# Kernel tuning notes

Measured on AMD Instinct MI355X. Metric: run time of the kernel, lower is better.

The kernel has to match this reference:

```python
import jax, jax.numpy as jnp
import numpy as np

B, T, D, FC, H = 256, 256, 512, 512, 512
EPS = 1e-5

def setup_inputs() -> dict:
    key = jax.random.key(0)
    ks = jax.random.split(key, 13)
    s = lambda k, shape, fan: jax.random.normal(k, shape, jnp.float32) * (1.0 / np.sqrt(fan))
    return {
        "inputs": jax.random.normal(ks[0], (B, T, D), jnp.float32),
        "hidden_state": jax.random.normal(ks[1], (B, H), jnp.float32),
        "episode_starts": jax.random.randint(ks[2], (B, T), 0, 2, jnp.int32),
        "ln_gamma": jnp.ones((D,), jnp.float32),
        "ln_beta": jnp.zeros((D,), jnp.float32),
        "w_in": s(ks[3], (FC, D), D),
        "b_in": jnp.zeros((FC,), jnp.float32),
        "w_ih": s(ks[4], (3 * H, FC), FC),
        "b_ih": jnp.zeros((3 * H,), jnp.float32),
        "w_hh": s(ks[5], (3 * H, H), H),
        "b_hh": jnp.zeros((3 * H,), jnp.float32),
        "w_out": s(ks[6], (H, H), H),
        "b_out": jnp.zeros((H,), jnp.float32),
    }

def reference(inputs, hidden_state, episode_starts, ln_gamma, ln_beta,
              w_in, b_in, w_ih, b_ih, w_hh, b_hh, w_out, b_out):
    # LayerNorm + fc_in + input-side GRU gates have no recurrence -> batch over time.
    mu = jnp.mean(inputs, axis=-1, keepdims=True)
    var = jnp.mean(jnp.square(inputs - mu), axis=-1, keepdims=True)
    xn = (inputs - mu) * jax.lax.rsqrt(var + EPS) * ln_gamma + ln_beta
    x = jax.nn.relu(jnp.einsum('btd,fd->btf', xn, w_in) + b_in)        # [B,T,FC]
    gi = jnp.einsum('btf,gf->btg', x, w_ih) + b_ih                      # [B,T,3H]
    mask = 1.0 - episode_starts.astype(jnp.float32)                     # [B,T]

    def step(h, inp):
        gi_t, m_t = inp                    # gi_t: [B,3H], m_t: [B]
        h = h * m_t[:, None]               # masked reset
        gh = h @ w_hh.T + b_hh             # [B,3H]
        ir, iz, inn = jnp.split(gi_t, 3, axis=-1)
        hr, hz, hn = jnp.split(gh, 3, axis=-1)
        r = jax.nn.sigmoid(ir + hr)
        z = jax.nn.sigmoid(iz + hz)
        n = jnp.tanh(inn + r * hn)
        h_new = (1.0 - z) * n + z * h
        return h_new, h_new

    h_last, hs = jax.lax.scan(step, hidden_state,
                              (gi.transpose(1, 0, 2), mask.T))          # hs: [T,B,H]
    outputs = jax.nn.relu(jnp.einsum('tbh,oh->tbo', hs, w_out) + b_out)
    return outputs.transpose(1, 0, 2), h_last
```

## Files before the change

### kernel.cpp

```cpp
#include <hip/hip_runtime.h>
#include <hip/hip_bf16.h>

#define B_  256
#define T_  256
#define D_  512
#define H_  512
#define G3_ 1536

typedef __attribute__((ext_vector_type(8))) short bf16x8;
typedef __attribute__((ext_vector_type(4))) float f32x4;
typedef __attribute__((ext_vector_type(8))) unsigned short u16x8;
typedef __attribute__((ext_vector_type(4))) unsigned short u16x4;

__device__ inline void gload_lds16(const void* g, void* l) {
  __builtin_amdgcn_global_load_lds((const __attribute__((address_space(1))) void*)g,
                                   (__attribute__((address_space(3))) void*)l,
                                   16, 0, 0);
}

__device__ inline unsigned short f2bu(float f) {
  __hip_bfloat16 h = __float2bfloat16(f);
  return *reinterpret_cast<unsigned short*>(&h);
}
__device__ inline float bu2f(unsigned short u) {
  return __uint_as_float((unsigned)u << 16);
}

__device__ inline bf16x8 ld16_sys(const void* p) {
  bf16x8 r;
  asm volatile("global_load_dwordx4 %0, %1, off sc0 sc1" : "=v"(r) : "v"(p) : "memory");
  return r;
}
__device__ inline void st8_sys(void* p, u16x4 v) {
  asm volatile("global_store_dwordx2 %0, %1, off sc0 sc1" :: "v"(p), "v"(v) : "memory");
}
__device__ inline void st4_sys(void* p, unsigned v) {
  asm volatile("global_store_dword %0, %1, off sc0 sc1" :: "v"(p), "v"(v) : "memory");
}
__device__ inline unsigned ld4_sys_wait(const void* p) {
  unsigned r;
  asm volatile("global_load_dword %0, %1, off sc0 sc1\n\ts_waitcnt vmcnt(0)"
               : "=v"(r) : "v"(p) : "memory");
  return r;
}
__device__ inline void waitvm0() { asm volatile("s_waitcnt vmcnt(0)" ::: "memory"); }

__global__ void prep_kernel(const float* __restrict__ w_in, const float* __restrict__ w_ih,
                            const float* __restrict__ w_out,
                            __hip_bfloat16* __restrict__ wib, __hip_bfloat16* __restrict__ whb,
                            __hip_bfloat16* __restrict__ wob, unsigned int* __restrict__ ctrs) {
  int i = blockIdx.x * 256 + threadIdx.x;
  if (i < D_ * D_)  wib[i] = __float2bfloat16(w_in[i]);
  if (i < G3_ * D_) whb[i] = __float2bfloat16(w_ih[i]);
  if (i < H_ * H_)  wob[i] = __float2bfloat16(w_out[i]);
  if (i < 1024) ctrs[i] = 0u;
}

__global__ __launch_bounds__(512) void ln_kernel(const float* __restrict__ x,
                                                 const float* __restrict__ gamma,
                                                 const float* __restrict__ beta,
                                                 __hip_bfloat16* __restrict__ xn) {
  long row = (long)blockIdx.x * 8 + (threadIdx.x >> 6);
  int lane = threadIdx.x & 63;
  const float4* rp = (const float4*)(x + row * D_ + lane * 8);
  float4 v0 = rp[0], v1 = rp[1];
  float s  = v0.x + v0.y + v0.z + v0.w + v1.x + v1.y + v1.z + v1.w;
  float sq = v0.x*v0.x + v0.y*v0.y + v0.z*v0.z + v0.w*v0.w
           + v1.x*v1.x + v1.y*v1.y + v1.z*v1.z + v1.w*v1.w;
  #pragma unroll
  for (int off = 1; off < 64; off <<= 1) { s += __shfl_xor(s, off); sq += __shfl_xor(sq, off); }
  float mean = s * (1.0f / D_);
  float var  = sq * (1.0f / D_) - mean * mean;
  float rstd = rsqrtf(var + 1e-5f);
  const float4* gp = (const float4*)(gamma + lane * 8);
  const float4* bp = (const float4*)(beta + lane * 8);
  float4 g0 = gp[0], g1 = gp[1], bb0 = bp[0], bb1 = bp[1];
  float vv[8] = {v0.x, v0.y, v0.z, v0.w, v1.x, v1.y, v1.z, v1.w};
  float gg[8] = {g0.x, g0.y, g0.z, g0.w, g1.x, g1.y, g1.z, g1.w};
  float bt[8] = {bb0.x, bb0.y, bb0.z, bb0.w, bb1.x, bb1.y, bb1.z, bb1.w};
  u16x8 ov;
  #pragma unroll
  for (int i = 0; i < 8; ++i) ov[i] = f2bu((vv[i] - mean) * rstd * gg[i] + bt[i]);
  *(u16x8*)(xn + row * D_ + lane * 8) = ov;
}

template<int ACT, int OUTBF>
__global__ __launch_bounds__(256) void gemm_bt(const __hip_bfloat16* __restrict__ A,
                                               const __hip_bfloat16* __restrict__ W,
                                               const float* __restrict__ bias,
                                               void* __restrict__ Cout,
                                               int M, int N, int K) {
  __shared__ __hip_bfloat16 As[128 * 64];
  __shared__ __hip_bfloat16 Ws[128 * 64];
  int tid  = threadIdx.x;
  int lane = tid & 63;
  int wave = tid >> 6;
  long row0 = (long)blockIdx.y * 128;
  long col0 = (long)blockIdx.x * 128;
  int qm = (wave >> 1) * 64, qn = (wave & 1) * 64;
  int lr = lane & 15, lk = (lane >> 4) * 8;
  f32x4 acc[4][4];
  #pragma unroll
  for (int mt = 0; mt < 4; ++mt)
    #pragma unroll
    for (int nt = 0; nt < 4; ++nt) acc[mt][nt] = {0.f, 0.f, 0.f, 0.f};

  for (int k0 = 0; k0 < K; k0 += 64) {
    #pragma unroll
    for (int i = 0; i < 4; ++i) {
      int e = i * 2048 + tid * 8;
      int r = e >> 6, c = e & 63;
      gload_lds16(A + (row0 + r) * K + k0 + c, (char*)As + 2 * e);
      gload_lds16(W + (col0 + r) * K + k0 + c, (char*)Ws + 2 * e);
    }
    __syncthreads();
    #pragma unroll
    for (int kc = 0; kc < 2; ++kc) {
      int kb = kc * 32 + lk;
      bf16x8 af[4], wf[4];
      #pragma unroll
      for (int mt = 0; mt < 4; ++mt) af[mt] = *(const bf16x8*)&As[(qm + mt * 16 + lr) * 64 + kb];
      #pragma unroll
      for (int nt = 0; nt < 4; ++nt) wf[nt] = *(const bf16x8*)&Ws[(qn + nt * 16 + lr) * 64 + kb];
      #pragma unroll
      for (int mt = 0; mt < 4; ++mt)
        #pragma unroll
        for (int nt = 0; nt < 4; ++nt)
          acc[mt][nt] = __builtin_amdgcn_mfma_f32_16x16x32_bf16(af[mt], wf[nt], acc[mt][nt], 0, 0, 0);
    }
    __syncthreads();
  }
  int r0 = (lane >> 4) * 4;
  #pragma unroll
  for (int nt = 0; nt < 4; ++nt) {
    long col = col0 + qn + nt * 16 + lr;
    float bv = bias[col];
    #pragma unroll
    for (int mt = 0; mt < 4; ++mt) {
      #pragma unroll
      for (int q = 0; q < 4; ++q) {
        long row = row0 + qm + mt * 16 + r0 + q;
        float v = acc[mt][nt][q] + bv;
        if (ACT) v = fmaxf(v, 0.0f);
        if (OUTBF) ((__hip_bfloat16*)Cout)[row * N + col] = __float2bfloat16(v);
        else       ((float*)Cout)[row * N + col] = v;
      }
    }
  }
}

__global__ __launch_bounds__(256) void scan_kernel(const __hip_bfloat16* __restrict__ gi,
                                                   const float* __restrict__ hidden,
                                                   const int* __restrict__ ep,
                                                   const float* __restrict__ w_hh,
                                                   const float* __restrict__ b_hh,
                                                   __hip_bfloat16* __restrict__ hs,
                                                   __hip_bfloat16* __restrict__ hbuf,
                                                   float* __restrict__ h_last,
                                                   unsigned int* __restrict__ flags) {
  __shared__ __hip_bfloat16 Wl[96][520];
  __shared__ float ghs[32][100];
  __shared__ f32x4 hown4[256];
  __shared__ unsigned epm[256];
  __shared__ float bhh[96];

  const int tid = threadIdx.x;
  const int bg = blockIdx.x & 7;
  const int nb = blockIdx.x >> 3;
  const int rb0 = bg * 32;
  const int j0 = nb * 32;
  unsigned* gflags = flags + bg * 16;

  for (int idx = tid; idx < 96 * 512; idx += 256) {
    int row = idx >> 9, c = idx & 511;
    int g = row >> 5, jj = row & 31;
    Wl[row][c] = __float2bfloat16(w_hh[(size_t)(g * 512 + j0 + jj) * 512 + c]);
  }
  if (tid < 96) bhh[tid] = b_hh[(tid >> 5) * 512 + j0 + (tid & 31)];
  {
    unsigned m = 0;
    for (int b = 0; b < 32; ++b)
      m |= (ep[(rb0 + b) * T_ + tid] != 0) ? (1u << b) : 0u;
    epm[tid] = m;
  }

  {
    int b = tid >> 3, jb = (tid & 7) * 4;
    const float4 hv = *(const float4*)(hidden + (size_t)(rb0 + b) * 512 + j0 + jb);
    f32x4 h4 = {hv.x, hv.y, hv.z, hv.w};
    hown4[tid] = h4;
    u16x4 hb;
    #pragma unroll
    for (int k = 0; k < 4; ++k) hb[k] = f2bu(h4[k]);
    st8_sys(hbuf + (size_t)(bg * 2) * 32 * 512 + b * 512 + j0 + jb, hb);
  }
  waitvm0();
  __syncthreads();
  if (tid == 0) st4_sys(gflags + nb, 1u);

  const int lane = tid & 63;
  const int wave = tid >> 6;
  const int mt = wave >> 1;
  const int npair = wave & 1;
  const int lr = lane & 15;
  const int asub = lane >> 4;
  const int arow = mt * 16 + lr;
  const int gb = tid >> 3, gjb = (tid & 7) * 4;

  for (int t = 0; t < T_; ++t) {
    const u16x4* gp = (const u16x4*)(gi + ((size_t)(rb0 + gb) * T_ + t) * G3_ + j0 + gjb);
    u16x4 gr4 = gp[0], gz4 = gp[128], gn4 = gp[256];

    if (wave == 0) {
      unsigned want = (unsigned)(t + 1);
      for (;;) {
        unsigned f = ld4_sys_wait(gflags + (lane & 15));
        if (__all((int)(f >= want))) break;
        __builtin_amdgcn_s_sleep(1);
      }
    }
    __syncthreads();

    const __hip_bfloat16* hsrc = hbuf + (size_t)(bg * 2 + (t & 1)) * 32 * 512;
    const char* abase = (const char*)(hsrc + (size_t)arow * 512 + asub * 8);
    bf16x8 af[16];
    #pragma unroll
    for (int kc = 0; kc < 16; ++kc) af[kc] = ld16_sys(abase + kc * 64);
    bool masked = ((epm[t] >> arow) & 1u) != 0u;
    waitvm0();
    __builtin_amdgcn_sched_barrier(0);
    if (masked) {
      #pragma unroll
      for (int kc = 0; kc < 16; ++kc) af[kc] = (bf16x8){0, 0, 0, 0, 0, 0, 0, 0};
    }

    f32x4 acc[3];
    #pragma unroll
    for (int i = 0; i < 3; ++i) acc[i] = (f32x4){0.f, 0.f, 0.f, 0.f};
    #pragma unroll
    for (int kc = 0; kc < 16; ++kc) {
      #pragma unroll
      for (int i = 0; i < 3; ++i) {
        bf16x8 bf = *(const bf16x8*)&Wl[npair * 48 + i * 16 + lr][kc * 32 + asub * 8];
        acc[i] = __builtin_amdgcn_mfma_f32_16x16x32_bf16(af[kc], bf, acc[i], 0, 0, 0);
      }
    }
    #pragma unroll
    for (int i = 0; i < 3; ++i)
      #pragma unroll
      for (int q = 0; q < 4; ++q)
        ghs[mt * 16 + asub * 4 + q][npair * 48 + i * 16 + lr] = acc[i][q];
    __syncthreads();

    __hip_bfloat16* hdst = hbuf + (size_t)(bg * 2 + ((t + 1) & 1)) * 32 * 512;
    unsigned em = epm[t];
    float live = ((em >> gb) & 1u) ? 0.0f : 1.0f;
    f32x4 ghr = *(const f32x4*)&ghs[gb][gjb];
    f32x4 ghz = *(const f32x4*)&ghs[gb][32 + gjb];
    f32x4 ghn = *(const f32x4*)&ghs[gb][64 + gjb];
    f32x4 hprev = hown4[tid];
    f32x4 hnew;
    u16x4 hb;
    #pragma unroll
    for (int k = 0; k < 4; ++k) {
      float r = 1.0f / (1.0f + __expf(-(bu2f(gr4[k]) + ghr[k] + bhh[gjb + k])));
      float z = 1.0f / (1.0f + __expf(-(bu2f(gz4[k]) + ghz[k] + bhh[32 + gjb + k])));
      float nx = bu2f(gn4[k]) + r * (ghn[k] + bhh[64 + gjb + k]);
      float n = 1.0f - 2.0f / (__expf(2.0f * nx) + 1.0f);
      float hp = hprev[k] * live;
      float hv = (1.0f - z) * n + z * hp;
      hnew[k] = hv;
      hb[k] = f2bu(hv);
    }
    hown4[tid] = hnew;
    *(u16x4*)&hs[((size_t)(rb0 + gb) * T_ + t) * 512 + j0 + gjb] = hb;
    st8_sys(hdst + gb * 512 + j0 + gjb, hb);
    waitvm0();
    __syncthreads();
    if (tid == 0) st4_sys(gflags + nb, (unsigned)(t + 2));
  }

  {
    int b = tid >> 3, jb = (tid & 7) * 4;
    f32x4 h4 = hown4[tid];
    *(float4*)(h_last + (size_t)(rb0 + b) * 512 + j0 + jb) = {h4[0], h4[1], h4[2], h4[3]};
  }
}

extern "C" void kernel_launch(void* const* d_in, const int* in_sizes, int n_in,
                              void* d_out, int out_size, void* d_ws, size_t ws_size,
                              hipStream_t stream) {
  const float* inputs = (const float*)d_in[0];
  const float* hidden = (const float*)d_in[1];
  const int*   ep     = (const int*)d_in[2];
  const float* gamma  = (const float*)d_in[3];
  const float* beta   = (const float*)d_in[4];
  const float* w_in   = (const float*)d_in[5];
  const float* b_in   = (const float*)d_in[6];
  const float* w_ih   = (const float*)d_in[7];
  const float* b_ih   = (const float*)d_in[8];
  const float* w_hh   = (const float*)d_in[9];
  const float* b_hh   = (const float*)d_in[10];
  const float* w_out  = (const float*)d_in[11];
  const float* b_out  = (const float*)d_in[12];

  char* ws = (char*)d_ws;
  size_t off = 0;
  auto alloc = [&](size_t bytes) { char* p = ws + off; off += (bytes + 255) & ~(size_t)255; return p; };
  const size_t BT = (size_t)B_ * T_;
  __hip_bfloat16* xn   = (__hip_bfloat16*)alloc(BT * D_ * 2);
  __hip_bfloat16* x    = (__hip_bfloat16*)alloc(BT * D_ * 2);
  __hip_bfloat16* gi   = (__hip_bfloat16*)alloc(BT * G3_ * 2);
  __hip_bfloat16* wib  = (__hip_bfloat16*)alloc((size_t)D_ * D_ * 2);
  __hip_bfloat16* whb  = (__hip_bfloat16*)alloc((size_t)G3_ * D_ * 2);
  __hip_bfloat16* wob  = (__hip_bfloat16*)alloc((size_t)H_ * H_ * 2);
  __hip_bfloat16* hbuf = (__hip_bfloat16*)alloc((size_t)8 * 2 * 32 * 512 * 2);
  unsigned int*   ctrs = (unsigned int*)alloc(4096);

  float* out    = (float*)d_out;
  float* h_last = out + BT * H_;

  prep_kernel<<<3072, 256, 0, stream>>>(w_in, w_ih, w_out, wib, whb, wob, ctrs);
  ln_kernel<<<B_ * T_ / 8, 512, 0, stream>>>(inputs, gamma, beta, xn);
  gemm_bt<1, 1><<<dim3(D_ / 128, BT / 128), 256, 0, stream>>>(xn, wib, b_in, x, BT, D_, D_);
  gemm_bt<0, 1><<<dim3(G3_ / 128, BT / 128), 256, 0, stream>>>(x, whb, b_ih, gi, BT, G3_, D_);
  __hip_bfloat16* hs = xn;
  scan_kernel<<<128, 256, 0, stream>>>(gi, hidden, ep, w_hh, b_hh, hs, hbuf, h_last, ctrs);
  gemm_bt<1, 0><<<dim3(H_ / 128, BT / 128), 256, 0, stream>>>(hs, wob, b_out, d_out, BT, H_, H_);
}
```

Baseline: 1.825 ms.

## Use per-wave flags in GRU scan, drop block barriers, prefetch gates

The cross-block handshake in the recurrent scan moves from one flag per block to one flag per wave. Every wave now polls all 64 flags of its batch group itself, which removes the leading and trailing __syncthreads of each timestep and the s_sleep backoff. The hidden state stays in registers instead of LDS, the bias values are hoisted into registers, and the next timestep's input-gate values are prefetched after the flag is published. The risks are heavier polling traffic on the flags, a flags buffer that must now hold four times as many entries, and correctness of reusing the ghs scratch without a closing block barrier.

```diff
diff --git a/kernel.cpp b/kernel.cpp
--- a/kernel.cpp
+++ b/kernel.cpp
@@ -160,23 +160,22 @@
                                                    unsigned int* __restrict__ flags) {
   __shared__ __hip_bfloat16 Wl[96][520];
   __shared__ float ghs[32][100];
-  __shared__ f32x4 hown4[256];
   __shared__ unsigned epm[256];
-  __shared__ float bhh[96];
+  __shared__ float bhhs[96];
 
   const int tid = threadIdx.x;
   const int bg = blockIdx.x & 7;
   const int nb = blockIdx.x >> 3;
   const int rb0 = bg * 32;
   const int j0 = nb * 32;
-  unsigned* gflags = flags + bg * 16;
+  unsigned* gflags = flags + bg * 64;
 
   for (int idx = tid; idx < 96 * 512; idx += 256) {
     int row = idx >> 9, c = idx & 511;
     int g = row >> 5, jj = row & 31;
     Wl[row][c] = __float2bfloat16(w_hh[(size_t)(g * 512 + j0 + jj) * 512 + c]);
   }
-  if (tid < 96) bhh[tid] = b_hh[(tid >> 5) * 512 + j0 + (tid & 31)];
+  if (tid < 96) bhhs[tid] = b_hh[(tid >> 5) * 512 + j0 + (tid & 31)];
   {
     unsigned m = 0;
     for (int b = 0; b < 32; ++b)
@@ -184,52 +183,60 @@
     epm[tid] = m;
   }
 
-  {
-    int b = tid >> 3, jb = (tid & 7) * 4;
-    const float4 hv = *(const float4*)(hidden + (size_t)(rb0 + b) * 512 + j0 + jb);
-    f32x4 h4 = {hv.x, hv.y, hv.z, hv.w};
-    hown4[tid] = h4;
-    u16x4 hb;
-    #pragma unroll
-    for (int k = 0; k < 4; ++k) hb[k] = f2bu(h4[k]);
-    st8_sys(hbuf + (size_t)(bg * 2) * 32 * 512 + b * 512 + j0 + jb, hb);
-  }
-  waitvm0();
-  __syncthreads();
-  if (tid == 0) st4_sys(gflags + nb, 1u);
-
   const int lane = tid & 63;
   const int wave = tid >> 6;
+  const int gb = tid >> 3, gjb = (tid & 7) * 4;
+
+  f32x4 hreg;
+  {
+    const float4 hv = *(const float4*)(hidden + (size_t)(rb0 + gb) * 512 + j0 + gjb);
+    hreg = (f32x4){hv.x, hv.y, hv.z, hv.w};
+    u16x4 hb;
+    #pragma unroll
+    for (int k = 0; k < 4; ++k) hb[k] = f2bu(hreg[k]);
+    st8_sys(hbuf + (size_t)(bg * 2) * 32 * 512 + gb * 512 + j0 + gjb, hb);
+  }
+  waitvm0();
+  if (lane == 0) st4_sys(gflags + nb * 4 + wave, 1u);
+  __syncthreads();
+
   const int mt = wave >> 1;
   const int npair = wave & 1;
   const int lr = lane & 15;
   const int asub = lane >> 4;
   const int arow = mt * 16 + lr;
-  const int gb = tid >> 3, gjb = (tid & 7) * 4;
+
+  float br_[4], bz_[4], bn_[4];
+  #pragma unroll
+  for (int k = 0; k < 4; ++k) {
+    br_[k] = bhhs[gjb + k];
+    bz_[k] = bhhs[32 + gjb + k];
+    bn_[k] = bhhs[64 + gjb + k];
+  }
+
+  const __hip_bfloat16* gibase = gi + (size_t)(rb0 + gb) * T_ * G3_ + j0 + gjb;
+  u16x4 gr4 = *(const u16x4*)(gibase);
+  u16x4 gz4 = *(const u16x4*)(gibase + 512);
+  u16x4 gn4 = *(const u16x4*)(gibase + 1024);
 
   for (int t = 0; t < T_; ++t) {
-    const u16x4* gp = (const u16x4*)(gi + ((size_t)(rb0 + gb) * T_ + t) * G3_ + j0 + gjb);
-    u16x4 gr4 = gp[0], gz4 = gp[128], gn4 = gp[256];
-
-    if (wave == 0) {
+    {
       unsigned want = (unsigned)(t + 1);
       for (;;) {
-        unsigned f = ld4_sys_wait(gflags + (lane & 15));
+        unsigned f = ld4_sys_wait(gflags + lane);
         if (__all((int)(f >= want))) break;
-        __builtin_amdgcn_s_sleep(1);
       }
     }
-    __syncthreads();
 
     const __hip_bfloat16* hsrc = hbuf + (size_t)(bg * 2 + (t & 1)) * 32 * 512;
     const char* abase = (const char*)(hsrc + (size_t)arow * 512 + asub * 8);
     bf16x8 af[16];
     #pragma unroll
     for (int kc = 0; kc < 16; ++kc) af[kc] = ld16_sys(abase + kc * 64);
-    bool masked = ((epm[t] >> arow) & 1u) != 0u;
+    bool maskd = ((epm[t] >> arow) & 1u) != 0u;
     waitvm0();
     __builtin_amdgcn_sched_barrier(0);
-    if (masked) {
+    if (maskd) {
       #pragma unroll
       for (int kc = 0; kc < 16; ++kc) af[kc] = (bf16x8){0, 0, 0, 0, 0, 0, 0, 0};
     }
@@ -253,38 +260,37 @@
     __syncthreads();
 
     __hip_bfloat16* hdst = hbuf + (size_t)(bg * 2 + ((t + 1) & 1)) * 32 * 512;
-    unsigned em = epm[t];
-    float live = ((em >> gb) & 1u) ? 0.0f : 1.0f;
+    float live = ((epm[t] >> gb) & 1u) ? 0.0f : 1.0f;
     f32x4 ghr = *(const f32x4*)&ghs[gb][gjb];
     f32x4 ghz = *(const f32x4*)&ghs[gb][32 + gjb];
     f32x4 ghn = *(const f32x4*)&ghs[gb][64 + gjb];
-    f32x4 hprev = hown4[tid];
     f32x4 hnew;
     u16x4 hb;
     #pragma unroll
     for (int k = 0; k < 4; ++k) {
-      float r = 1.0f / (1.0f + __expf(-(bu2f(gr4[k]) + ghr[k] + bhh[gjb + k])));
-      float z = 1.0f / (1.0f + __expf(-(bu2f(gz4[k]) + ghz[k] + bhh[32 + gjb + k])));
-      float nx = bu2f(gn4[k]) + r * (ghn[k] + bhh[64 + gjb + k]);
+      float r = 1.0f / (1.0f + __expf(-(bu2f(gr4[k]) + ghr[k] + br_[k])));
+      float z = 1.0f / (1.0f + __expf(-(bu2f(gz4[k]) + ghz[k] + bz_[k])));
+      float nx = bu2f(gn4[k]) + r * (ghn[k] + bn_[k]);
       float n = 1.0f - 2.0f / (__expf(2.0f * nx) + 1.0f);
-      float hp = hprev[k] * live;
+      float hp = hreg[k] * live;
       float hv = (1.0f - z) * n + z * hp;
       hnew[k] = hv;
       hb[k] = f2bu(hv);
     }
-    hown4[tid] = hnew;
-    *(u16x4*)&hs[((size_t)(rb0 + gb) * T_ + t) * 512 + j0 + gjb] = hb;
     st8_sys(hdst + gb * 512 + j0 + gjb, hb);
     waitvm0();
-    __syncthreads();
-    if (tid == 0) st4_sys(gflags + nb, (unsigned)(t + 2));
-  }
-
-  {
-    int b = tid >> 3, jb = (tid & 7) * 4;
-    f32x4 h4 = hown4[tid];
-    *(float4*)(h_last + (size_t)(rb0 + b) * 512 + j0 + jb) = {h4[0], h4[1], h4[2], h4[3]};
-  }
+    if (lane == 0) st4_sys(gflags + nb * 4 + wave, (unsigned)(t + 2));
+
+    int tn = (t + 1 < T_) ? (t + 1) : t;
+    gr4 = *(const u16x4*)(gibase + (size_t)tn * G3_);
+    gz4 = *(const u16x4*)(gibase + (size_t)tn * G3_ + 512);
+    gn4 = *(const u16x4*)(gibase + (size_t)tn * G3_ + 1024);
+    *(u16x4*)&hs[((size_t)(rb0 + gb) * T_ + t) * 512 + j0 + gjb] = hb;
+    hreg = hnew;
+  }
+
+  *(float4*)(h_last + (size_t)(rb0 + gb) * 512 + j0 + gjb) =
+      (float4){hreg[0], hreg[1], hreg[2], hreg[3]};
 }
 
 extern "C" void kernel_launch(void* const* d_in, const int* in_sizes, int n_in,
```

Result: slower. 2.409 ms (+32.0%).
